# Performance work log

Measured on AMD Instinct MI355X. Metric: run time of the kernel, lower is better.

The kernel has to match this reference:

```python
import jax, jax.numpy as jnp
import numpy as np

N = 100_000   # nodes
E = 1_600_000  # edges (avg degree 16)
D_IN, D_HID, D_OUT = 128, 128, 64


def setup_inputs() -> dict:
    key = jax.random.key(0)
    k = jax.random.split(key, 6)
    x = jax.random.normal(k[0], (N, D_IN), dtype=jnp.float32)
    edge_index = jax.random.randint(k[1], (2, E), 0, N, dtype=jnp.int32)
    W1 = jax.random.normal(k[2], (D_IN, D_HID), dtype=jnp.float32) / np.sqrt(D_IN)
    b1 = jnp.zeros((D_HID,), dtype=jnp.float32)
    W2 = jax.random.normal(k[3], (D_HID, D_OUT), dtype=jnp.float32) / np.sqrt(D_HID)
    b2 = jnp.zeros((D_OUT,), dtype=jnp.float32)
    return {"x": x, "edge_index": edge_index, "W1": W1, "b1": b1, "W2": W2, "b2": b2}


def reference(x, edge_index, W1, b1, W2, b2):
    # GCNConv (PyG defaults): add self-loops, symmetric deg^-1/2 normalization,
    # linear transform then sum-aggregate over neighbors, then bias.
    loop = jnp.arange(N, dtype=edge_index.dtype)
    src = jnp.concatenate([edge_index[0], loop])  # [E+N]
    dst = jnp.concatenate([edge_index[1], loop])  # [E+N]

    deg = jax.ops.segment_sum(jnp.ones(src.shape, jnp.float32), dst, num_segments=N)
    inv_sqrt_deg = jnp.where(deg > 0, jax.lax.rsqrt(jnp.maximum(deg, 1.0)), 0.0)
    coef = (inv_sqrt_deg[src] * inv_sqrt_deg[dst])[:, None]  # [E+N, 1]

    def gcn_conv(h, W, b):
        h = h @ W                                   # [N, d_out]
        msg = h[src] * coef                          # gather + scale, [E+N, d_out]
        return jax.ops.segment_sum(msg, dst, num_segments=N) + b

    h = jax.nn.relu(gcn_conv(x, W1, b1))
    # dropout is identity in eval mode
    return gcn_conv(h, W2, b2)
```

## Files before the change

### kernel.cpp

```cpp
#include <hip/hip_runtime.h>

#define NN 100000
#define NE 1600000
#define DI 128
#define DH 128
#define DO 64
#define NN16 ((size_t)NN * 16)
#define NBK 391
#define SLOT 5120
#define PAD 16
#define EPB 8192
#define NSB ((NE + EPB - 1) / EPB)

typedef unsigned int uint;
typedef unsigned short ushort;
typedef __bf16 bf16x8 __attribute__((ext_vector_type(8)));
typedef float f32x4 __attribute__((ext_vector_type(4)));

__device__ __forceinline__ float bf_lo(uint u) { return __uint_as_float(u << 16); }
__device__ __forceinline__ float bf_hi(uint u) { return __uint_as_float(u & 0xffff0000u); }
__device__ __forceinline__ ushort f2bf(float f) {
    uint u = __float_as_uint(f);
    uint r = u + 0x7fffu + ((u >> 16) & 1u);
    return (ushort)(r >> 16);
}

__global__ void k_prep(const float* __restrict__ W1, const float* __restrict__ W2,
                       ushort* __restrict__ w1t, ushort* __restrict__ w2t,
                       int* __restrict__ bcur) {
    int t = blockIdx.x * 256 + threadIdx.x;
    if (t < NBK) bcur[t * PAD] = t * SLOT;
    if (t < 128 * 128) {
        int c = t >> 7, k = t & 127;
        w1t[t] = f2bf(W1[k * 128 + c]);
    } else if (t < 128 * 128 + 64 * 128) {
        int u = t - 128 * 128;
        int c = u >> 7, k = u & 127;
        w2t[u] = f2bf(W2[k * 64 + c]);
    }
}

__global__ __launch_bounds__(512) void k_bscatter(const int* __restrict__ src,
                                                  const int* __restrict__ dst,
                                                  int* __restrict__ bcur,
                                                  uint* __restrict__ ebuf) {
    __shared__ uint stage[EPB];
    __shared__ ushort bktid[EPB];
    __shared__ int lcnt[NBK];
    __shared__ int loff[NBK];
    __shared__ int gbase[NBK];
    __shared__ int s[512];
    int t = threadIdx.x;
    int e0 = blockIdx.x * EPB;
    int n = min(EPB, NE - e0);
    for (int i = t; i < NBK; i += 512) lcnt[i] = 0;
    __syncthreads();
    for (int i = t; i < n; i += 512)
        atomicAdd(&lcnt[dst[e0 + i] >> 8], 1);
    __syncthreads();
    int myc = (t < NBK) ? lcnt[t] : 0;
    s[t] = myc;
    __syncthreads();
    for (int d = 1; d < 512; d <<= 1) {
        int a = (t >= d) ? s[t - d] : 0;
        __syncthreads();
        s[t] += a;
        __syncthreads();
    }
    if (t < NBK) {
        loff[t] = s[t] - myc;
        gbase[t] = atomicAdd(&bcur[t * PAD], myc);
        lcnt[t] = s[t] - myc;
    }
    __syncthreads();
    for (int i = t; i < n; i += 512) {
        int d = dst[e0 + i];
        int sv = src[e0 + i];
        int b = d >> 8;
        int p = atomicAdd(&lcnt[b], 1);
        stage[p] = ((uint)sv << 8) | (uint)(d & 255);
        bktid[p] = (ushort)b;
    }
    __syncthreads();
    for (int j = t; j < n; j += 512) {
        int b = bktid[j];
        ebuf[gbase[b] + (j - loff[b])] = stage[j];
    }
}

__global__ __launch_bounds__(256) void k_bfill(const uint* __restrict__ ebuf,
                                               const int* __restrict__ bcur,
                                               uint2* __restrict__ offdeg,
                                               float* __restrict__ inv,
                                               int* __restrict__ csr_src) {
    __shared__ int cnt[256];
    __shared__ int s[256];
    __shared__ int cur[256];
    int b = blockIdx.x, t = threadIdx.x;
    int ebeg = b * SLOT;
    int eend = bcur[b * PAD];
    cnt[t] = 0;
    __syncthreads();
    for (int e = ebeg + t; e < eend; e += 256)
        atomicAdd(&cnt[ebuf[e] & 255], 1);
    __syncthreads();
    int v = cnt[t];
    s[t] = v;
    __syncthreads();
    for (int d = 1; d < 256; d <<= 1) {
        int a = (t >= d) ? s[t - d] : 0;
        __syncthreads();
        s[t] += a;
        __syncthreads();
    }
    int beg = ebeg + s[t] - v;
    int node = b * 256 + t;
    if (node < NN) {
        offdeg[node] = make_uint2((uint)beg, (uint)v);
        inv[node] = rsqrtf((float)v + 1.0f);
    }
    cur[t] = beg;
    __syncthreads();
    for (int e = ebeg + t; e < eend; e += 256) {
        uint ed = ebuf[e];
        int p = atomicAdd(&cur[ed & 255], 1);
        csr_src[p] = (int)(ed >> 8);
    }
}

template <int N, bool ABF16>
__global__ __launch_bounds__(256) void k_gemm_mfma(const void* __restrict__ Ap,
                                                   const ushort* __restrict__ Wt,
                                                   const float* __restrict__ inv,
                                                   ushort* __restrict__ out) {
    int wid = threadIdx.x >> 6;
    int lane = threadIdx.x & 63;
    int r0 = (blockIdx.x * 4 + wid) * 32;
    if (r0 >= NN) return;
    int rlo = lane & 15, khi = lane >> 4;

    constexpr int CT = N / 16;
    f32x4 acc[2][CT] = {};

#pragma unroll
    for (int ks = 0; ks < 4; ++ks) {
        bf16x8 bf[CT];
#pragma unroll
        for (int ct = 0; ct < CT; ++ct)
            bf[ct] = *(const bf16x8*)(Wt + (ct * 16 + rlo) * 128 + ks * 32 + khi * 8);
#pragma unroll
        for (int rt = 0; rt < 2; ++rt) {
            int row = r0 + rt * 16 + rlo;
            bf16x8 af;
            if (ABF16) {
                const ushort* As = (const ushort*)Ap;
                af = *(const bf16x8*)(As + (size_t)(2 * ks + (khi >> 1)) * NN16 +
                                      (size_t)row * 16 + (khi & 1) * 8);
            } else {
                const float* pa = (const float*)Ap + (size_t)row * 128 + ks * 32 + khi * 8;
                float4 f0 = *(const float4*)pa;
                float4 f1 = *(const float4*)(pa + 4);
                af[0] = (__bf16)f0.x; af[1] = (__bf16)f0.y;
                af[2] = (__bf16)f0.z; af[3] = (__bf16)f0.w;
                af[4] = (__bf16)f1.x; af[5] = (__bf16)f1.y;
                af[6] = (__bf16)f1.z; af[7] = (__bf16)f1.w;
            }
#pragma unroll
            for (int ct = 0; ct < CT; ++ct)
                acc[rt][ct] = __builtin_amdgcn_mfma_f32_16x16x32_bf16(af, bf[ct], acc[rt][ct], 0, 0, 0);
        }
    }
#pragma unroll
    for (int rt = 0; rt < 2; ++rt) {
        int rowb = r0 + rt * 16 + 4 * khi;
#pragma unroll
        for (int b = 0; b < 4; ++b) {
            float sc = inv[rowb + b];
#pragma unroll
            for (int ct = 0; ct < CT; ++ct)
                out[(size_t)ct * NN16 + (size_t)(rowb + b) * 16 + rlo] = f2bf(acc[rt][ct][b] * sc);
        }
    }
}

template <int NS, bool RELU, bool F32OUT>
__global__ __launch_bounds__(256) void k_aggs(const uint2* __restrict__ offdeg,
                                              const int* __restrict__ csr,
                                              const ushort* __restrict__ tab,
                                              const float* __restrict__ inv,
                                              const float* __restrict__ bias,
                                              void* __restrict__ outp) {
    int slice = blockIdx.x & (NS - 1);
    int nb = blockIdx.x / NS;
    int lane = threadIdx.x & 63;
    int wid = threadIdx.x >> 6;
    int g = lane >> 3;
    int u = lane & 7;
    const uint* t32 = (const uint*)tab + (size_t)slice * (NN * 8);
    float2 bb = *(const float2*)(bias + slice * 16 + u * 2);
#pragma unroll
    for (int j = 0; j < 8; ++j) {
        int node = nb * 256 + wid * 64 + j * 8 + g;
        if (node >= NN) continue;
        uint2 od = offdeg[node];
        int beg = (int)od.x, deg = (int)od.y;
        float a0 = 0.f, a1 = 0.f;
        int full = deg & ~7;
        int r = 0;
        for (; r < full; r += 8) {
            int sidx = csr[beg + r + u];
#pragma unroll
            for (int e = 0; e < 8; ++e) {
                int se = __shfl(sidx, (g << 3) + e);
                uint uu = t32[(size_t)se * 8 + u];
                a0 += bf_lo(uu); a1 += bf_hi(uu);
            }
        }
        int rem = deg - full;
        if (rem) {
            int sidx = csr[beg + min(r + u, deg - 1)];
#pragma unroll
            for (int e = 0; e < 8; ++e) {
                if (e < rem) {
                    int se = __shfl(sidx, (g << 3) + e);
                    uint uu = t32[(size_t)se * 8 + u];
                    a0 += bf_lo(uu); a1 += bf_hi(uu);
                }
            }
        }
        uint su = t32[(size_t)node * 8 + u];
        a0 += bf_lo(su); a1 += bf_hi(su);
        float invd = inv[node];
        float r0 = fmaf(invd, a0, bb.x);
        float r1 = fmaf(invd, a1, bb.y);
        if (RELU) { r0 = fmaxf(r0, 0.f); r1 = fmaxf(r1, 0.f); }
        if (F32OUT) {
            float* out = (float*)outp;
            *(float2*)(out + (size_t)node * 64 + slice * 16 + u * 2) = make_float2(r0, r1);
        } else {
            uint* o32 = (uint*)outp + (size_t)slice * (NN * 8);
            o32[(size_t)node * 8 + u] = (uint)f2bf(r0) | ((uint)f2bf(r1) << 16);
        }
    }
}

extern "C" void kernel_launch(void* const* d_in, const int* in_sizes, int n_in,
                              void* d_out, int out_size, void* d_ws, size_t ws_size,
                              hipStream_t stream) {
    const float* x  = (const float*)d_in[0];
    const int* ei   = (const int*)d_in[1];
    const int* src  = ei;
    const int* dst  = ei + NE;
    const float* W1 = (const float*)d_in[2];
    const float* b1 = (const float*)d_in[3];
    const float* W2 = (const float*)d_in[4];
    const float* b2 = (const float*)d_in[5];
    float* out = (float*)d_out;

    uint2*  offdeg  = (uint2*)d_ws;
    float*  inv     = (float*)(offdeg + NN);
    int*    bcur    = (int*)(inv + 100004);
    int*    csr_src = bcur + NBK * PAD;
    ushort* w1t     = (ushort*)(csr_src + NBK * SLOT);
    ushort* w2t     = w1t + 128 * 128;
    ushort* h       = w2t + 64 * 128;
    ushort* hagg    = h + (size_t)NN * DH;
    ushort* h2      = hagg + (size_t)NN * DH;
    uint*   ebuf    = (uint*)h2;

    k_prep<<<96, 256, 0, stream>>>(W1, W2, w1t, w2t, bcur);
    k_bscatter<<<NSB, 512, 0, stream>>>(src, dst, bcur, ebuf);
    k_bfill<<<NBK, 256, 0, stream>>>(ebuf, bcur, offdeg, inv, csr_src);

    k_gemm_mfma<DH, false><<<(NN + 127) / 128, 256, 0, stream>>>(x, w1t, inv, h);
    k_aggs<8, true, false><<<NBK * 8, 256, 0, stream>>>(offdeg, csr_src, h, inv, b1, hagg);

    k_gemm_mfma<DO, true><<<(NN + 127) / 128, 256, 0, stream>>>(hagg, w2t, inv, h2);
    k_aggs<4, false, true><<<NBK * 4, 256, 0, stream>>>(offdeg, csr_src, h2, inv, b2, out);
}
```

Before: 246.7 us.

## Aggregate one node per wave with edge-parallel lanes and fold prep into bfill

The aggregation kernel now assigns one node per wavefront, with eight edge groups of eight lanes loading neighbors in parallel and a shuffle-xor reduction at the end, instead of eight nodes per wave each walking edges serially. This is meant to expose more memory-level parallelism per node and reduce the serial latency chain on low-degree nodes. The separate prep kernel is replaced by a memset plus weight conversion folded into k_bfill, with bucket offsets made relative. The trade-off is far more blocks, only one lane-group in eight doing output writes, and lanes sitting idle when a node has few edges.

```diff
diff --git a/kernel.cpp b/kernel.cpp
--- a/kernel.cpp
+++ b/kernel.cpp
@@ -23,21 +23,6 @@
     uint u = __float_as_uint(f);
     uint r = u + 0x7fffu + ((u >> 16) & 1u);
     return (ushort)(r >> 16);
-}
-
-__global__ void k_prep(const float* __restrict__ W1, const float* __restrict__ W2,
-                       ushort* __restrict__ w1t, ushort* __restrict__ w2t,
-                       int* __restrict__ bcur) {
-    int t = blockIdx.x * 256 + threadIdx.x;
-    if (t < NBK) bcur[t * PAD] = t * SLOT;
-    if (t < 128 * 128) {
-        int c = t >> 7, k = t & 127;
-        w1t[t] = f2bf(W1[k * 128 + c]);
-    } else if (t < 128 * 128 + 64 * 128) {
-        int u = t - 128 * 128;
-        int c = u >> 7, k = u & 127;
-        w2t[u] = f2bf(W2[k * 64 + c]);
-    }
 }
 
 __global__ __launch_bounds__(512) void k_bscatter(const int* __restrict__ src,
@@ -69,7 +54,7 @@
     }
     if (t < NBK) {
         loff[t] = s[t] - myc;
-        gbase[t] = atomicAdd(&bcur[t * PAD], myc);
+        gbase[t] = t * SLOT + atomicAdd(&bcur[t * PAD], myc);
         lcnt[t] = s[t] - myc;
     }
     __syncthreads();
@@ -92,13 +77,28 @@
                                                const int* __restrict__ bcur,
                                                uint2* __restrict__ offdeg,
                                                float* __restrict__ inv,
-                                               int* __restrict__ csr_src) {
+                                               int* __restrict__ csr_src,
+                                               const float* __restrict__ W1,
+                                               const float* __restrict__ W2,
+                                               ushort* __restrict__ w1t,
+                                               ushort* __restrict__ w2t) {
     __shared__ int cnt[256];
     __shared__ int s[256];
     __shared__ int cur[256];
     int b = blockIdx.x, t = threadIdx.x;
+    {
+        int g = b * 256 + t;
+        if (g < 128 * 128) {
+            int c = g >> 7, k = g & 127;
+            w1t[g] = f2bf(W1[k * 128 + c]);
+        } else if (g < 128 * 128 + 64 * 128) {
+            int u = g - 128 * 128;
+            int c = u >> 7, k = u & 127;
+            w2t[u] = f2bf(W2[k * 64 + c]);
+        }
+    }
     int ebeg = b * SLOT;
-    int eend = bcur[b * PAD];
+    int eend = ebeg + bcur[b * PAD];
     cnt[t] = 0;
     __syncthreads();
     for (int e = ebeg + t; e < eend; e += 256)
@@ -184,7 +184,7 @@
 }
 
 template <int NS, bool RELU, bool F32OUT>
-__global__ __launch_bounds__(256) void k_aggs(const uint2* __restrict__ offdeg,
+__global__ __launch_bounds__(256) void k_aggv(const uint2* __restrict__ offdeg,
                                               const int* __restrict__ csr,
                                               const ushort* __restrict__ tab,
                                               const float* __restrict__ inv,
@@ -192,54 +192,47 @@
                                               void* __restrict__ outp) {
     int slice = blockIdx.x & (NS - 1);
     int nb = blockIdx.x / NS;
-    int lane = threadIdx.x & 63;
-    int wid = threadIdx.x >> 6;
-    int g = lane >> 3;
-    int u = lane & 7;
+    int wid = threadIdx.x >> 6, lane = threadIdx.x & 63;
+    int e8 = lane >> 3, u = lane & 7;
+    int node = nb * 4 + wid;
+    if (node >= NN) return;
+    uint2 od = offdeg[node];
+    int beg = (int)od.x, deg = (int)od.y;
     const uint* t32 = (const uint*)tab + (size_t)slice * (NN * 8);
-    float2 bb = *(const float2*)(bias + slice * 16 + u * 2);
-#pragma unroll
-    for (int j = 0; j < 8; ++j) {
-        int node = nb * 256 + wid * 64 + j * 8 + g;
-        if (node >= NN) continue;
-        uint2 od = offdeg[node];
-        int beg = (int)od.x, deg = (int)od.y;
-        float a0 = 0.f, a1 = 0.f;
-        int full = deg & ~7;
-        int r = 0;
-        for (; r < full; r += 8) {
-            int sidx = csr[beg + r + u];
-#pragma unroll
-            for (int e = 0; e < 8; ++e) {
-                int se = __shfl(sidx, (g << 3) + e);
-                uint uu = t32[(size_t)se * 8 + u];
-                a0 += bf_lo(uu); a1 += bf_hi(uu);
-            }
-        }
-        int rem = deg - full;
-        if (rem) {
-            int sidx = csr[beg + min(r + u, deg - 1)];
-#pragma unroll
-            for (int e = 0; e < 8; ++e) {
-                if (e < rem) {
-                    int se = __shfl(sidx, (g << 3) + e);
-                    uint uu = t32[(size_t)se * 8 + u];
-                    a0 += bf_lo(uu); a1 += bf_hi(uu);
-                }
-            }
-        }
+    float a0 = 0.f, a1 = 0.f;
+    int r = 0;
+    for (; r + 16 <= deg; r += 16) {
+        int s0 = csr[beg + r + e8];
+        int s1 = csr[beg + r + 8 + e8];
+        uint u0 = t32[(size_t)s0 * 8 + u];
+        uint u1 = t32[(size_t)s1 * 8 + u];
+        a0 += bf_lo(u0); a1 += bf_hi(u0);
+        a0 += bf_lo(u1); a1 += bf_hi(u1);
+    }
+    for (; r < deg; r += 8) {
+        int e = r + e8;
+        if (e < deg) {
+            int s = csr[beg + e];
+            uint uu = t32[(size_t)s * 8 + u];
+            a0 += bf_lo(uu); a1 += bf_hi(uu);
+        }
+    }
+    a0 += __shfl_xor(a0, 8);  a1 += __shfl_xor(a1, 8);
+    a0 += __shfl_xor(a0, 16); a1 += __shfl_xor(a1, 16);
+    a0 += __shfl_xor(a0, 32); a1 += __shfl_xor(a1, 32);
+    if (e8 == 0) {
+        float invd = inv[node];
         uint su = t32[(size_t)node * 8 + u];
-        a0 += bf_lo(su); a1 += bf_hi(su);
-        float invd = inv[node];
-        float r0 = fmaf(invd, a0, bb.x);
-        float r1 = fmaf(invd, a1, bb.y);
+        float2 bb = *(const float2*)(bias + slice * 16 + u * 2);
+        float r0 = fmaf(invd, a0 + bf_lo(su), bb.x);
+        float r1 = fmaf(invd, a1 + bf_hi(su), bb.y);
         if (RELU) { r0 = fmaxf(r0, 0.f); r1 = fmaxf(r1, 0.f); }
         if (F32OUT) {
-            float* out = (float*)outp;
-            *(float2*)(out + (size_t)node * 64 + slice * 16 + u * 2) = make_float2(r0, r1);
+            float* o = (float*)outp + (size_t)node * 64 + slice * 16 + u * 2;
+            *(float2*)o = make_float2(r0, r1);
         } else {
-            uint* o32 = (uint*)outp + (size_t)slice * (NN * 8);
-            o32[(size_t)node * 8 + u] = (uint)f2bf(r0) | ((uint)f2bf(r1) << 16);
+            uint* o32 = (uint*)outp + (size_t)slice * (NN * 8) + (size_t)node * 8 + u;
+            *o32 = (uint)f2bf(r0) | ((uint)f2bf(r1) << 16);
         }
     }
 }
@@ -268,13 +261,13 @@
     ushort* h2      = hagg + (size_t)NN * DH;
     uint*   ebuf    = (uint*)h2;
 
-    k_prep<<<96, 256, 0, stream>>>(W1, W2, w1t, w2t, bcur);
+    hipMemsetAsync(bcur, 0, (size_t)NBK * PAD * sizeof(int), stream);
     k_bscatter<<<NSB, 512, 0, stream>>>(src, dst, bcur, ebuf);
-    k_bfill<<<NBK, 256, 0, stream>>>(ebuf, bcur, offdeg, inv, csr_src);
+    k_bfill<<<NBK, 256, 0, stream>>>(ebuf, bcur, offdeg, inv, csr_src, W1, W2, w1t, w2t);
 
     k_gemm_mfma<DH, false><<<(NN + 127) / 128, 256, 0, stream>>>(x, w1t, inv, h);
-    k_aggs<8, true, false><<<NBK * 8, 256, 0, stream>>>(offdeg, csr_src, h, inv, b1, hagg);
+    k_aggv<8, true, false><<<((NN + 3) / 4) * 8, 256, 0, stream>>>(offdeg, csr_src, h, inv, b1, hagg);
 
     k_gemm_mfma<DO, true><<<(NN + 127) / 128, 256, 0, stream>>>(hagg, w2t, inv, h2);
-    k_aggs<4, false, true><<<NBK * 4, 256, 0, stream>>>(offdeg, csr_src, h2, inv, b2, out);
-}
+    k_aggv<4, false, true><<<((NN + 3) / 4) * 4, 256, 0, stream>>>(offdeg, csr_src, h2, inv, b2, out);
+}
```

After: 410.7 us. +66.4%, slower.
